# Kernel optimization log

Measured on AMD Instinct MI355X. Metric: run time of the kernel, lower is better.

The kernel has to match this reference:

```python
import jax, jax.numpy as jnp
import numpy as np

D_MODEL = 128
D_HIDDEN = 256
D_STATE = 16
EXPAND = 2
D_INNER = EXPAND * D_MODEL  # 256
DT_RANK = (D_MODEL + 15) // 16  # 8, mamba_ssm default ceil(d_model/16)
N = 8192  # decoded reads (sequence length for Mamba)
M = 8192  # encoded reads


def setup_inputs() -> dict:
    key = jax.random.key(0)
    ks = jax.random.split(key, 16)
    s = 0.02
    return {
        "encoded_reads": jax.random.normal(ks[0], (M, D_MODEL), jnp.float32),
        "decoded_reads": jax.random.normal(ks[1], (N, D_MODEL), jnp.float32),
        # Mamba block params (d_conv=1 -> depthwise conv is per-channel affine)
        "in_proj_w": jax.random.normal(ks[2], (2 * D_INNER, D_MODEL), jnp.float32) * s,
        "conv_w": jax.random.normal(ks[3], (D_INNER,), jnp.float32) * s + 1.0,
        "conv_b": jnp.zeros((D_INNER,), jnp.float32),
        "x_proj_w": jax.random.normal(ks[4], (DT_RANK + 2 * D_STATE, D_INNER), jnp.float32) * s,
        "dt_proj_w": jax.random.normal(ks[5], (D_INNER, DT_RANK), jnp.float32) * s,
        "dt_proj_b": jnp.full((D_INNER,), -4.0, jnp.float32),  # softplus(-4)~0.018, typical dt init
        "A_log": jnp.log(jnp.broadcast_to(jnp.arange(1, D_STATE + 1, dtype=jnp.float32), (D_INNER, D_STATE))),
        "D": jnp.ones((D_INNER,), jnp.float32),
        "out_proj_w": jax.random.normal(ks[6], (D_MODEL, D_INNER), jnp.float32) * s,
        # query/key projections (nn.Linear with bias)
        "q_w": jax.random.normal(ks[7], (D_HIDDEN, D_MODEL), jnp.float32) * s,
        "q_b": jnp.zeros((D_HIDDEN,), jnp.float32),
        "k_w": jax.random.normal(ks[8], (D_HIDDEN, D_MODEL), jnp.float32) * s,
        "k_b": jnp.zeros((D_HIDDEN,), jnp.float32),
    }


def _mamba(u, in_proj_w, conv_w, conv_b, x_proj_w, dt_proj_w, dt_proj_b, A_log, D, out_proj_w):
    # u: [L, d_model] treated as a single sequence
    xz = u @ in_proj_w.T                         # [L, 2*d_inner]
    x, z = jnp.split(xz, 2, axis=-1)             # [L, d_inner] each
    # depthwise conv1d with kernel size 1 == per-channel affine, then SiLU
    x = jax.nn.silu(x * conv_w + conv_b)
    x_dbl = x @ x_proj_w.T                       # [L, dt_rank + 2*d_state]
    dt, B, C = jnp.split(x_dbl, [DT_RANK, DT_RANK + D_STATE], axis=-1)
    dt = jax.nn.softplus(dt @ dt_proj_w.T + dt_proj_b)  # [L, d_inner]
    A = -jnp.exp(A_log)                          # [d_inner, d_state]
    deltaA = jnp.exp(dt[:, :, None] * A)         # [L, d_inner, d_state]
    deltaBx = dt[:, :, None] * B[:, None, :] * x[:, :, None]  # [L, d_inner, d_state]

    def step(h, inp):
        dA_t, dBx_t, C_t = inp
        h = dA_t * h + dBx_t                     # [d_inner, d_state]
        y_t = jnp.einsum('dn,n->d', h, C_t)      # [d_inner]
        return h, y_t

    h0 = jnp.zeros((D_INNER, D_STATE), x.dtype)
    _, y = jax.lax.scan(step, h0, (deltaA, deltaBx, C))  # y: [L, d_inner]
    y = (y + D * x) * jax.nn.silu(z)
    return y @ out_proj_w.T                      # [L, d_model]


def reference(encoded_reads, decoded_reads, in_proj_w, conv_w, conv_b, x_proj_w,
              dt_proj_w, dt_proj_b, A_log, D, out_proj_w, q_w, q_b, k_w, k_b):
    decoded_processed = _mamba(decoded_reads, in_proj_w, conv_w, conv_b, x_proj_w,
                               dt_proj_w, dt_proj_b, A_log, D, out_proj_w)
    queries = decoded_processed @ q_w.T + q_b    # [N, d_hidden]
    keys = encoded_reads @ k_w.T + k_b           # [M, d_hidden]
    scores = jnp.einsum('nd,md->nm', queries, keys)
    return jax.nn.softmax(scores, axis=-1)
```

## Files before the change

### kernel.cpp

```cpp
#include <hip/hip_runtime.h>
#include <hip/hip_bf16.h>

typedef __attribute__((ext_vector_type(8))) short bf16x8;
typedef __attribute__((ext_vector_type(4))) float f32x4;

#define CHUNK 32
#define NCHUNK 256

__device__ __forceinline__ void gload16(const void* g, void* l) {
    __builtin_amdgcn_global_load_lds(
        (const __attribute__((address_space(1))) void*)g,
        (__attribute__((address_space(3))) void*)l,
        16, 0, 0);
}

__device__ __forceinline__ float silu_f(float v) { return v / (1.0f + __expf(-v)); }

__global__ __launch_bounds__(256) void prep_k(
    const float* __restrict__ in_proj_w, const float* __restrict__ x_proj_w,
    const float* __restrict__ k_w, const float* __restrict__ q_w,
    const float* __restrict__ out_proj_w,
    __hip_bfloat16* __restrict__ wib, __hip_bfloat16* __restrict__ wxb,
    __hip_bfloat16* __restrict__ kwb, __hip_bfloat16* __restrict__ wcb)
{
    const int b = blockIdx.x, t = threadIdx.x;
    if (b < 424) {
        int idx = b * 256 + t;
        if (idx < 65536)      wib[idx]         = __float2bfloat16(in_proj_w[idx]);
        else if (idx < 75776) wxb[idx - 65536] = __float2bfloat16(x_proj_w[idx - 65536]);
        else                  kwb[idx - 75776] = __float2bfloat16(k_w[idx - 75776]);
    } else {
        const int hh = b - 424;
        float acc = 0.0f;
        for (int m = 0; m < 128; ++m) acc += q_w[hh * 128 + m] * out_proj_w[m * 256 + t];
        wcb[hh * 256 + t] = __float2bfloat16(acc);
    }
}

template<int OUT_BF16, int HAS_BIAS>
__global__ __launch_bounds__(256) void gemm_bt_k(
    const __hip_bfloat16* __restrict__ A,
    const __hip_bfloat16* __restrict__ B,
    float* __restrict__ Cf, __hip_bfloat16* __restrict__ Cb,
    const float* __restrict__ bias, int M, int N, int K)
{
    __shared__ __hip_bfloat16 As[64][40];
    __shared__ __hip_bfloat16 Bs[64][40];
    const int tid  = threadIdx.x;
    const int wave = tid >> 6;
    const int lane = tid & 63;
    const int wm = (wave >> 1) << 5;
    const int wn = (wave & 1) << 5;
    const long bm = (long)blockIdx.y << 6;
    const long bn = (long)blockIdx.x << 6;

    f32x4 acc[2][2] = {{{0.f,0.f,0.f,0.f},{0.f,0.f,0.f,0.f}},
                       {{0.f,0.f,0.f,0.f},{0.f,0.f,0.f,0.f}}};

    const int sr = tid >> 2;
    const int sc = (tid & 3) << 3;
    const int lr = lane & 15;
    const int kg = (lane >> 4) << 3;

    for (int k0 = 0; k0 < K; k0 += 32) {
        {
            long ar = bm + sr;
            bf16x8 av = {0,0,0,0,0,0,0,0};
            if (ar < M) av = *(const bf16x8*)(A + ar * K + k0 + sc);
            *(bf16x8*)&As[sr][sc] = av;
            long br = bn + sr;
            bf16x8 bv = {0,0,0,0,0,0,0,0};
            if (br < N) bv = *(const bf16x8*)(B + br * K + k0 + sc);
            *(bf16x8*)&Bs[sr][sc] = bv;
        }
        __syncthreads();
        bf16x8 a0 = *(const bf16x8*)&As[wm + lr][kg];
        bf16x8 a1 = *(const bf16x8*)&As[wm + 16 + lr][kg];
        bf16x8 b0 = *(const bf16x8*)&Bs[wn + lr][kg];
        bf16x8 b1 = *(const bf16x8*)&Bs[wn + 16 + lr][kg];
        acc[0][0] = __builtin_amdgcn_mfma_f32_16x16x32_bf16(a0, b0, acc[0][0], 0, 0, 0);
        acc[0][1] = __builtin_amdgcn_mfma_f32_16x16x32_bf16(a0, b1, acc[0][1], 0, 0, 0);
        acc[1][0] = __builtin_amdgcn_mfma_f32_16x16x32_bf16(a1, b0, acc[1][0], 0, 0, 0);
        acc[1][1] = __builtin_amdgcn_mfma_f32_16x16x32_bf16(a1, b1, acc[1][1], 0, 0, 0);
        __syncthreads();
    }
    const int rg = (lane >> 4) << 2;
    #pragma unroll
    for (int i = 0; i < 2; ++i)
      #pragma unroll
      for (int j = 0; j < 2; ++j)
        #pragma unroll
        for (int r = 0; r < 4; ++r) {
            long row = bm + wm + i * 16 + rg + r;
            long col = bn + wn + j * 16 + lr;
            if (row < M && col < N) {
                float v = acc[i][j][r];
                if (HAS_BIAS) v += bias[col];
                if (OUT_BF16) Cb[row * N + col] = __float2bfloat16(v);
                else          Cf[row * N + col] = v;
            }
        }
}

template<int EPI>
__global__ __launch_bounds__(256) void gemm_f32a_k(
    const float* __restrict__ A, const __hip_bfloat16* __restrict__ B,
    const float* __restrict__ w0, const float* __restrict__ w1,
    float* __restrict__ xf, __hip_bfloat16* __restrict__ ob, float* __restrict__ zs,
    int M, int N, int K)
{
    __shared__ __hip_bfloat16 As[64][40];
    __shared__ __hip_bfloat16 Bs[64][40];
    const int tid  = threadIdx.x;
    const int wave = tid >> 6;
    const int lane = tid & 63;
    const int wm = (wave >> 1) << 5;
    const int wn = (wave & 1) << 5;
    const long bm = (long)blockIdx.y << 6;
    const long bn = (long)blockIdx.x << 6;

    f32x4 acc[2][2] = {{{0.f,0.f,0.f,0.f},{0.f,0.f,0.f,0.f}},
                       {{0.f,0.f,0.f,0.f},{0.f,0.f,0.f,0.f}}};

    const int sr = tid >> 2;
    const int sc = (tid & 3) << 3;
    const int lr = lane & 15;
    const int kg = (lane >> 4) << 3;

    for (int k0 = 0; k0 < K; k0 += 32) {
        {
            long ar = bm + sr;
            f32x4 x0 = *(const f32x4*)(A + ar * K + k0 + sc);
            f32x4 x1 = *(const f32x4*)(A + ar * K + k0 + sc + 4);
            union { bf16x8 v; __hip_bfloat16 h[8]; } u;
            u.h[0] = __float2bfloat16(x0[0]); u.h[1] = __float2bfloat16(x0[1]);
            u.h[2] = __float2bfloat16(x0[2]); u.h[3] = __float2bfloat16(x0[3]);
            u.h[4] = __float2bfloat16(x1[0]); u.h[5] = __float2bfloat16(x1[1]);
            u.h[6] = __float2bfloat16(x1[2]); u.h[7] = __float2bfloat16(x1[3]);
            *(bf16x8*)&As[sr][sc] = u.v;
            long br = bn + sr;
            bf16x8 bv = {0,0,0,0,0,0,0,0};
            if (br < N) bv = *(const bf16x8*)(B + br * K + k0 + sc);
            *(bf16x8*)&Bs[sr][sc] = bv;
        }
        __syncthreads();
        bf16x8 a0 = *(const bf16x8*)&As[wm + lr][kg];
        bf16x8 a1 = *(const bf16x8*)&As[wm + 16 + lr][kg];
        bf16x8 b0 = *(const bf16x8*)&Bs[wn + lr][kg];
        bf16x8 b1 = *(const bf16x8*)&Bs[wn + 16 + lr][kg];
        acc[0][0] = __builtin_amdgcn_mfma_f32_16x16x32_bf16(a0, b0, acc[0][0], 0, 0, 0);
        acc[0][1] = __builtin_amdgcn_mfma_f32_16x16x32_bf16(a0, b1, acc[0][1], 0, 0, 0);
        acc[1][0] = __builtin_amdgcn_mfma_f32_16x16x32_bf16(a1, b0, acc[1][0], 0, 0, 0);
        acc[1][1] = __builtin_amdgcn_mfma_f32_16x16x32_bf16(a1, b1, acc[1][1], 0, 0, 0);
        __syncthreads();
    }
    const int rg = (lane >> 4) << 2;
    #pragma unroll
    for (int i = 0; i < 2; ++i)
      #pragma unroll
      for (int j = 0; j < 2; ++j)
        #pragma unroll
        for (int r = 0; r < 4; ++r) {
            long row = bm + wm + i * 16 + rg + r;
            long col = bn + wn + j * 16 + lr;
            float v = acc[i][j][r];
            if (EPI == 0) {
                if (col < 256) {
                    float xv = v * w0[col] + w1[col];
                    float s = silu_f(xv);
                    xf[row * 256 + col] = s;
                    ob[row * 256 + col] = __float2bfloat16(s);
                } else {
                    zs[row * 256 + col - 256] = silu_f(v);
                }
            } else {
                ob[row * N + col] = __float2bfloat16(v + w0[col]);
            }
        }
}

template<int PASS>
__global__ __launch_bounds__(256) void scores_k(
    const __hip_bfloat16* __restrict__ Q, const __hip_bfloat16* __restrict__ Kb,
    float* __restrict__ out, const float* __restrict__ invZ)
{
    __shared__ alignas(16) char Asb[128 * 128];
    __shared__ alignas(16) char Bsb[128 * 128];
    const int tid = threadIdx.x, wave = tid >> 6, lane = tid & 63;
    const int bm = blockIdx.y << 7, bn = blockIdx.x << 7;
    const int wm = (wave >> 1) << 6, wn = (wave & 1) << 6;
    const int K = 256;

    f32x4 acc[4][4];
    #pragma unroll
    for (int i = 0; i < 4; ++i)
      #pragma unroll
      for (int j = 0; j < 4; ++j)
        acc[i][j] = (f32x4){0.f, 0.f, 0.f, 0.f};

    for (int k0 = 0; k0 < 256; k0 += 64) {
        #pragma unroll
        for (int c = 0; c < 4; ++c) {
            const int base = (wave * 4 + c) * 1024;
            const int o = base + lane * 16;
            const int q = o ^ (((o >> 7) & 7) << 4);
            const int row = q >> 7, col = (q & 127) >> 1;
            gload16(Q  + (size_t)(bm + row) * K + k0 + col, Asb + base);
            gload16(Kb + (size_t)(bn + row) * K + k0 + col, Bsb + base);
        }
        __syncthreads();
        #pragma unroll
        for (int ks = 0; ks < 2; ++ks) {
            bf16x8 af[4], bfr[4];
            const int cb = ks * 64 + ((lane >> 4) << 4);
            #pragma unroll
            for (int i = 0; i < 4; ++i) {
                const int ra = wm + i * 16 + (lane & 15);
                af[i]  = *(const bf16x8*)(Asb + ((ra * 128 + cb) ^ ((ra & 7) << 4)));
                const int rb = wn + i * 16 + (lane & 15);
                bfr[i] = *(const bf16x8*)(Bsb + ((rb * 128 + cb) ^ ((rb & 7) << 4)));
            }
            #pragma unroll
            for (int i = 0; i < 4; ++i)
              #pragma unroll
              for (int j = 0; j < 4; ++j)
                acc[i][j] = __builtin_amdgcn_mfma_f32_16x16x32_bf16(af[i], bfr[j], acc[i][j], 0, 0, 0);
        }
        __syncthreads();
    }

    const int lr = lane & 15, rg = (lane >> 4) << 2;
    if (PASS == 0) {
        #pragma unroll
        for (int i = 0; i < 4; ++i) {
            #pragma unroll
            for (int r = 0; r < 4; ++r) {
                float s = __expf(acc[i][0][r]) + __expf(acc[i][1][r])
                        + __expf(acc[i][2][r]) + __expf(acc[i][3][r]);
                #pragma unroll
                for (int o = 1; o < 16; o <<= 1) s += __shfl_xor(s, o, 64);
                if (lr == 0)
                    out[(size_t)(blockIdx.x * 2 + (wave & 1)) * 8192
                        + bm + wm + i * 16 + rg + r] = s;
            }
        }
    } else {
        #pragma unroll
        for (int i = 0; i < 4; ++i)
          #pragma unroll
          for (int r = 0; r < 4; ++r) {
            const int row = bm + wm + i * 16 + rg + r;
            const float iz = invZ[row];
            #pragma unroll
            for (int j = 0; j < 4; ++j)
                __builtin_nontemporal_store(__expf(acc[i][j][r]) * iz,
                    out + (size_t)row * 8192 + bn + wn + j * 16 + lr);
          }
    }
}

__global__ __launch_bounds__(256) void rowsum_inv_k(
    const float* __restrict__ partial, float* __restrict__ invZ)
{
    const int row = blockIdx.x * 256 + threadIdx.x;
    float s = 0.0f;
    for (int c = 0; c < 128; ++c) s += partial[(size_t)c * 8192 + row];
    invZ[row] = 1.0f / s;
}

__global__ __launch_bounds__(256) void scan_chunk_k(
    const float* __restrict__ xf, const float* __restrict__ xdbl,
    const float* __restrict__ dtw, const float* __restrict__ dtb,
    const float* __restrict__ A_log,
    float* __restrict__ P, float* __restrict__ S)
{
    __shared__ float xs[CHUNK * 40];
    const int c = blockIdx.x, d = threadIdx.x;
    const int t0 = c * CHUNK;
    for (int k = d; k < CHUNK * 40; k += 256) xs[k] = xdbl[(size_t)t0 * 40 + k];
    __syncthreads();
    const f32x4 wa = *(const f32x4*)(dtw + d * 8);
    const f32x4 wb = *(const f32x4*)(dtw + d * 8 + 4);
    const float dbias = dtb[d];
    float An[16], Pv[16], Sv[16];
    #pragma unroll
    for (int n = 0; n < 16; ++n) { An[n] = -expf(A_log[d * 16 + n]); Pv[n] = 1.0f; Sv[n] = 0.0f; }
    for (int tt = 0; tt < CHUNK; ++tt) {
        const float* xr = xs + tt * 40;
        float dr = dbias + xr[0]*wa[0] + xr[1]*wa[1] + xr[2]*wa[2] + xr[3]*wa[3]
                         + xr[4]*wb[0] + xr[5]*wb[1] + xr[6]*wb[2] + xr[7]*wb[3];
        float dt = (dr > 20.0f) ? dr : logf(1.0f + expf(dr));
        float xv = xf[(size_t)(t0 + tt) * 256 + d];
        float dtx = dt * xv;
        #pragma unroll
        for (int n = 0; n < 16; ++n) {
            float a = __expf(dt * An[n]);
            Pv[n] *= a;
            Sv[n] = a * Sv[n] + dtx * xr[8 + n];
        }
    }
    size_t base = (size_t)c * 4096 + (size_t)d * 16;
    #pragma unroll
    for (int n = 0; n < 16; ++n) { P[base + n] = Pv[n]; S[base + n] = Sv[n]; }
}

__global__ __launch_bounds__(256) void scan_carry_k(
    const float* __restrict__ P, const float* __restrict__ S, float* __restrict__ hinit)
{
    const int ch = blockIdx.x * 256 + threadIdx.x;
    float h = 0.0f;
    for (int c = 0; c < NCHUNK; c += 8) {
        float p[8], s[8];
        #pragma unroll
        for (int j = 0; j < 8; ++j) {
            p[j] = P[(size_t)(c + j) * 4096 + ch];
            s[j] = S[(size_t)(c + j) * 4096 + ch];
        }
        #pragma unroll
        for (int j = 0; j < 8; ++j) {
            hinit[(size_t)(c + j) * 4096 + ch] = h;
            h = p[j] * h + s[j];
        }
    }
}

__global__ __launch_bounds__(256) void scan_final_k(
    const float* __restrict__ xf, const float* __restrict__ xdbl,
    const float* __restrict__ dtw, const float* __restrict__ dtb,
    const float* __restrict__ A_log, const float* __restrict__ hinit,
    const float* __restrict__ Dp, const float* __restrict__ zs,
    __hip_bfloat16* __restrict__ yfb)
{
    __shared__ float xs[CHUNK * 40];
    const int c = blockIdx.x, d = threadIdx.x;
    const int t0 = c * CHUNK;
    for (int k = d; k < CHUNK * 40; k += 256) xs[k] = xdbl[(size_t)t0 * 40 + k];
    __syncthreads();
    const f32x4 wa = *(const f32x4*)(dtw + d * 8);
    const f32x4 wb = *(const f32x4*)(dtw + d * 8 + 4);
    const float dbias = dtb[d];
    float An[16], h[16];
    #pragma unroll
    for (int n = 0; n < 16; ++n) {
        An[n] = -expf(A_log[d * 16 + n]);
        h[n] = hinit[(size_t)c * 4096 + (size_t)d * 16 + n];
    }
    const float Dv = Dp[d];
    for (int tt = 0; tt < CHUNK; ++tt) {
        const float* xr = xs + tt * 40;
        float dr = dbias + xr[0]*wa[0] + xr[1]*wa[1] + xr[2]*wa[2] + xr[3]*wa[3]
                         + xr[4]*wb[0] + xr[5]*wb[1] + xr[6]*wb[2] + xr[7]*wb[3];
        float dt = (dr > 20.0f) ? dr : logf(1.0f + expf(dr));
        float xv = xf[(size_t)(t0 + tt) * 256 + d];
        float dtx = dt * xv;
        float y = 0.0f;
        #pragma unroll
        for (int n = 0; n < 16; ++n) {
            float a = __expf(dt * An[n]);
            h[n] = a * h[n] + dtx * xr[8 + n];
            y += h[n] * xr[24 + n];
        }
        float outv = (y + Dv * xv) * zs[(size_t)(t0 + tt) * 256 + d];
        yfb[(size_t)(t0 + tt) * 256 + d] = __float2bfloat16(outv);
    }
}

extern "C" void kernel_launch(void* const* d_in, const int* in_sizes, int n_in,
                              void* d_out, int out_size, void* d_ws, size_t ws_size,
                              hipStream_t stream)
{
    const float* enc        = (const float*)d_in[0];
    const float* dec        = (const float*)d_in[1];
    const float* in_proj_w  = (const float*)d_in[2];
    const float* conv_w     = (const float*)d_in[3];
    const float* conv_b     = (const float*)d_in[4];
    const float* x_proj_w   = (const float*)d_in[5];
    const float* dt_proj_w  = (const float*)d_in[6];
    const float* dt_proj_b  = (const float*)d_in[7];
    const float* A_log      = (const float*)d_in[8];
    const float* Dp         = (const float*)d_in[9];
    const float* out_proj_w = (const float*)d_in[10];
    const float* q_w        = (const float*)d_in[11];
    const float* q_b        = (const float*)d_in[12];
    const float* k_w        = (const float*)d_in[13];
    const float* k_b        = (const float*)d_in[14];

    char* ws = (char*)d_ws;
    size_t off = 0;
    auto alloc = [&](size_t bytes) -> void* {
        void* p = ws + off;
        off += (bytes + 255) & ~(size_t)255;
        return p;
    };
    __hip_bfloat16* wib  = (__hip_bfloat16*)alloc((size_t)512 * 128 * 2);
    __hip_bfloat16* wxb  = (__hip_bfloat16*)alloc((size_t)40 * 256 * 2);
    __hip_bfloat16* kwb  = (__hip_bfloat16*)alloc((size_t)256 * 128 * 2);
    __hip_bfloat16* wcb  = (__hip_bfloat16*)alloc((size_t)256 * 256 * 2);
    float* xf    = (float*)alloc((size_t)8192 * 256 * 4);
    __hip_bfloat16* xb = (__hip_bfloat16*)alloc((size_t)8192 * 256 * 2);
    float* zs    = (float*)alloc((size_t)8192 * 256 * 4);
    float* xdbl  = (float*)alloc((size_t)8192 * 40 * 4);
    float* P     = (float*)alloc((size_t)NCHUNK * 4096 * 4);
    float* Ssum  = (float*)alloc((size_t)NCHUNK * 4096 * 4);
    float* hinit = (float*)alloc((size_t)NCHUNK * 4096 * 4);
    __hip_bfloat16* yfb = (__hip_bfloat16*)alloc((size_t)8192 * 256 * 2);
    __hip_bfloat16* qbm = (__hip_bfloat16*)alloc((size_t)8192 * 256 * 2);
    __hip_bfloat16* kbm = (__hip_bfloat16*)alloc((size_t)8192 * 256 * 2);
    float* partial = (float*)alloc((size_t)128 * 8192 * 4);
    float* invZ    = (float*)alloc((size_t)8192 * 4);
    (void)ws_size;

    prep_k<<<680, 256, 0, stream>>>(in_proj_w, x_proj_w, k_w, q_w, out_proj_w,
                                    wib, wxb, kwb, wcb);

    {
        dim3 g(512 / 64, 8192 / 64);
        gemm_f32a_k<0><<<g, 256, 0, stream>>>(dec, wib, conv_w, conv_b,
                                              xf, xb, zs, 8192, 512, 128);
    }
    {
        dim3 g(1, 8192 / 64);
        gemm_bt_k<0, 0><<<g, 256, 0, stream>>>(xb, wxb, xdbl, nullptr, nullptr, 8192, 40, 256);
    }
    scan_chunk_k<<<NCHUNK, 256, 0, stream>>>(xf, xdbl, dt_proj_w, dt_proj_b, A_log, P, Ssum);
    scan_carry_k<<<16, 256, 0, stream>>>(P, Ssum, hinit);
    scan_final_k<<<NCHUNK, 256, 0, stream>>>(xf, xdbl, dt_proj_w, dt_proj_b, A_log,
                                             hinit, Dp, zs, yfb);

    {
        dim3 g(256 / 64, 8192 / 64);
        gemm_bt_k<1, 1><<<g, 256, 0, stream>>>(yfb, wcb, nullptr, qbm, q_b, 8192, 256, 256);
    }
    {
        dim3 g(256 / 64, 8192 / 64);
        gemm_f32a_k<1><<<g, 256, 0, stream>>>(enc, kwb, k_b, nullptr,
                                              nullptr, kbm, nullptr, 8192, 256, 128);
    }

    {
        dim3 g(8192 / 128, 8192 / 128);
        scores_k<0><<<g, 256, 0, stream>>>(qbm, kbm, partial, nullptr);
        rowsum_inv_k<<<8192 / 256, 256, 0, stream>>>(partial, invZ);
        scores_k<1><<<g, 256, 0, stream>>>(qbm, kbm, (float*)d_out, invZ);
    }
}
```

Before: 237.2 us.

## Retile scores kernel to 256x256 blocks with double-buffered LDS pipeline

Each scores block now computes a 256x256 output tile with 512 threads instead of 128x128 with 256 threads, which doubles operand reuse per LDS load. The K loop is fully unrolled into a two-buffer pipeline that issues global-to-LDS loads one stage ahead, using explicit vmcnt/lgkmcnt waits, raw barriers and s_setprio around the MFMA sections. The row-sum partial layout is adapted so the reduction still sees 128 partial columns. The 128KB of LDS per block likely allows only one block per CU despite the launch bounds, and the larger accumulator array raises register pressure.

```diff
diff --git a/kernel.cpp b/kernel.cpp
--- a/kernel.cpp
+++ b/kernel.cpp
@@ -180,81 +180,111 @@
 }
 
 template<int PASS>
-__global__ __launch_bounds__(256) void scores_k(
+__global__ __launch_bounds__(512, 2) void scores_k(
     const __hip_bfloat16* __restrict__ Q, const __hip_bfloat16* __restrict__ Kb,
     float* __restrict__ out, const float* __restrict__ invZ)
 {
-    __shared__ alignas(16) char Asb[128 * 128];
-    __shared__ alignas(16) char Bsb[128 * 128];
+    __shared__ alignas(16) char lds[2][2][32768];
     const int tid = threadIdx.x, wave = tid >> 6, lane = tid & 63;
-    const int bm = blockIdx.y << 7, bn = blockIdx.x << 7;
-    const int wm = (wave >> 1) << 6, wn = (wave & 1) << 6;
+    const int bm = blockIdx.y << 8, bn = blockIdx.x << 8;
+    const int wr = wave >> 2, wc = wave & 3;
     const int K = 256;
 
-    f32x4 acc[4][4];
-    #pragma unroll
-    for (int i = 0; i < 4; ++i)
+    f32x4 acc[8][4];
+    #pragma unroll
+    for (int i = 0; i < 8; ++i)
       #pragma unroll
       for (int j = 0; j < 4; ++j)
         acc[i][j] = (f32x4){0.f, 0.f, 0.f, 0.f};
 
-    for (int k0 = 0; k0 < 256; k0 += 64) {
-        #pragma unroll
-        for (int c = 0; c < 4; ++c) {
-            const int base = (wave * 4 + c) * 1024;
-            const int o = base + lane * 16;
-            const int q = o ^ (((o >> 7) & 7) << 4);
-            const int row = q >> 7, col = (q & 127) >> 1;
-            gload16(Q  + (size_t)(bm + row) * K + k0 + col, Asb + base);
-            gload16(Kb + (size_t)(bn + row) * K + k0 + col, Bsb + base);
-        }
-        __syncthreads();
-        #pragma unroll
-        for (int ks = 0; ks < 2; ++ks) {
-            bf16x8 af[4], bfr[4];
-            const int cb = ks * 64 + ((lane >> 4) << 4);
-            #pragma unroll
-            for (int i = 0; i < 4; ++i) {
-                const int ra = wm + i * 16 + (lane & 15);
-                af[i]  = *(const bf16x8*)(Asb + ((ra * 128 + cb) ^ ((ra & 7) << 4)));
-                const int rb = wn + i * 16 + (lane & 15);
-                bfr[i] = *(const bf16x8*)(Bsb + ((rb * 128 + cb) ^ ((rb & 7) << 4)));
-            }
-            #pragma unroll
-            for (int i = 0; i < 4; ++i)
-              #pragma unroll
-              for (int j = 0; j < 4; ++j)
-                acc[i][j] = __builtin_amdgcn_mfma_f32_16x16x32_bf16(af[i], bfr[j], acc[i][j], 0, 0, 0);
-        }
-        __syncthreads();
-    }
-
-    const int lr = lane & 15, rg = (lane >> 4) << 2;
+    #define STAGE(buf, k0)                                                          \
+        { _Pragma("unroll")                                                         \
+          for (int is = 0; is < 4; ++is) {                                          \
+            const int o = (is * 512 + tid) * 16;                                    \
+            const int q = o ^ (((o >> 7) & 7) << 4);                                \
+            const int row = o >> 7;                                                 \
+            const int ce  = (q & 127) >> 1;                                         \
+            gload16(Q  + (size_t)(bm + row) * K + (k0) + ce, &lds[buf][0][o]);      \
+            gload16(Kb + (size_t)(bn + row) * K + (k0) + ce, &lds[buf][1][o]);      \
+          } }
+
+    #define COMPUTE(buf)                                                            \
+        { _Pragma("unroll")                                                         \
+          for (int ks = 0; ks < 2; ++ks) {                                          \
+            const int cb = ks * 64 + ((lane >> 4) << 4);                            \
+            bf16x8 bfr[4];                                                          \
+            _Pragma("unroll")                                                       \
+            for (int j = 0; j < 4; ++j) {                                           \
+                const int rb = wc * 64 + j * 16 + (lane & 15);                      \
+                bfr[j] = *(const bf16x8*)&lds[buf][1][(rb * 128 + cb) ^ ((rb & 7) << 4)]; \
+            }                                                                       \
+            _Pragma("unroll")                                                       \
+            for (int i = 0; i < 8; ++i) {                                           \
+                const int ra = wr * 128 + i * 16 + (lane & 15);                     \
+                bf16x8 af = *(const bf16x8*)&lds[buf][0][(ra * 128 + cb) ^ ((ra & 7) << 4)]; \
+                _Pragma("unroll")                                                   \
+                for (int j = 0; j < 4; ++j)                                         \
+                    acc[i][j] = __builtin_amdgcn_mfma_f32_16x16x32_bf16(af, bfr[j], acc[i][j], 0, 0, 0); \
+            } } }
+
+    STAGE(0, 0)
+    STAGE(1, 64)
+    asm volatile("s_waitcnt vmcnt(8)" ::: "memory");
+    __builtin_amdgcn_s_barrier();
+    __builtin_amdgcn_s_setprio(1);
+    COMPUTE(0)
+    __builtin_amdgcn_s_setprio(0);
+    asm volatile("s_waitcnt lgkmcnt(0)" ::: "memory");
+    __builtin_amdgcn_s_barrier();
+    STAGE(0, 128)
+    asm volatile("s_waitcnt vmcnt(8)" ::: "memory");
+    __builtin_amdgcn_s_barrier();
+    __builtin_amdgcn_s_setprio(1);
+    COMPUTE(1)
+    __builtin_amdgcn_s_setprio(0);
+    asm volatile("s_waitcnt lgkmcnt(0)" ::: "memory");
+    __builtin_amdgcn_s_barrier();
+    STAGE(1, 192)
+    asm volatile("s_waitcnt vmcnt(8)" ::: "memory");
+    __builtin_amdgcn_s_barrier();
+    __builtin_amdgcn_s_setprio(1);
+    COMPUTE(0)
+    __builtin_amdgcn_s_setprio(0);
+    asm volatile("s_waitcnt lgkmcnt(0)" ::: "memory");
+    __builtin_amdgcn_s_barrier();
+    asm volatile("s_waitcnt vmcnt(0)" ::: "memory");
+    __builtin_amdgcn_s_barrier();
+    __builtin_amdgcn_s_setprio(1);
+    COMPUTE(1)
+    __builtin_amdgcn_s_setprio(0);
+    #undef STAGE
+    #undef COMPUTE
+
+    const int lr = lane & 15, rg = (lane >> 4);
     if (PASS == 0) {
         #pragma unroll
-        for (int i = 0; i < 4; ++i) {
-            #pragma unroll
-            for (int r = 0; r < 4; ++r) {
-                float s = __expf(acc[i][0][r]) + __expf(acc[i][1][r])
-                        + __expf(acc[i][2][r]) + __expf(acc[i][3][r]);
-                #pragma unroll
-                for (int o = 1; o < 16; o <<= 1) s += __shfl_xor(s, o, 64);
-                if (lr == 0)
-                    out[(size_t)(blockIdx.x * 2 + (wave & 1)) * 8192
-                        + bm + wm + i * 16 + rg + r] = s;
-            }
-        }
-    } else {
-        #pragma unroll
-        for (int i = 0; i < 4; ++i)
+        for (int i = 0; i < 8; ++i)
           #pragma unroll
           for (int r = 0; r < 4; ++r) {
-            const int row = bm + wm + i * 16 + rg + r;
+            float s = __expf(acc[i][0][r]) + __expf(acc[i][1][r])
+                    + __expf(acc[i][2][r]) + __expf(acc[i][3][r]);
+            #pragma unroll
+            for (int o = 1; o < 16; o <<= 1) s += __shfl_xor(s, o, 64);
+            if (lr == 0)
+                out[(size_t)(blockIdx.x * 4 + wc) * 8192
+                    + bm + wr * 128 + i * 16 + rg * 4 + r] = s;
+          }
+    } else {
+        #pragma unroll
+        for (int i = 0; i < 8; ++i)
+          #pragma unroll
+          for (int r = 0; r < 4; ++r) {
+            const int row = bm + wr * 128 + i * 16 + rg * 4 + r;
             const float iz = invZ[row];
             #pragma unroll
             for (int j = 0; j < 4; ++j)
                 __builtin_nontemporal_store(__expf(acc[i][j][r]) * iz,
-                    out + (size_t)row * 8192 + bn + wn + j * 16 + lr);
+                    out + (size_t)row * 8192 + bn + wc * 64 + j * 16 + lr);
           }
     }
 }
@@ -438,9 +468,9 @@
     }
 
     {
-        dim3 g(8192 / 128, 8192 / 128);
-        scores_k<0><<<g, 256, 0, stream>>>(qbm, kbm, partial, nullptr);
+        dim3 g(8192 / 256, 8192 / 256);
+        scores_k<0><<<g, 512, 0, stream>>>(qbm, kbm, partial, nullptr);
         rowsum_inv_k<<<8192 / 256, 256, 0, stream>>>(partial, invZ);
-        scores_k<1><<<g, 256, 0, stream>>>(qbm, kbm, (float*)d_out, invZ);
-    }
-}
+        scores_k<1><<<g, 512, 0, stream>>>(qbm, kbm, (float*)d_out, invZ);
+    }
+}
```

Measured after the change: 264.5 us. +11.5%, slower.
